# Performance work log

Hardware: AMD Instinct MI355X
Metric: run time of the kernel (lower is better)

Reference implementation:

```python
import jax, jax.numpy as jnp
import numpy as np
import math

BS, SEQ, HID = 1, 2048, 2048
NH, NKV, HD = 32, 8, 64
BASE = 10000.0


def rotate_half(x):
    x1, x2 = x[..., : x.shape[-1] // 2], x[..., x.shape[-1] // 2 :]
    return jnp.concatenate((-x2, x1), axis=-1)


def setup_inputs() -> dict:
    key = jax.random.key(0)
    ks = jax.random.split(key, 6)
    s = 0.02
    return {
        "x": jax.random.normal(ks[0], (BS, SEQ, HID), dtype=jnp.float32),
        "attention_mask": jnp.zeros((BS, SEQ), dtype=jnp.float32),
        "position_ids": jnp.broadcast_to(jnp.arange(SEQ, dtype=jnp.int64 if jax.config.jax_enable_x64 else jnp.int32), (BS, SEQ)),
        "wq": jax.random.normal(ks[1], (HID, NH * HD), dtype=jnp.float32) * s,
        "wk": jax.random.normal(ks[2], (HID, NKV * HD), dtype=jnp.float32) * s,
        "wv": jax.random.normal(ks[3], (HID, NKV * HD), dtype=jnp.float32) * s,
        "wo": jax.random.normal(ks[4], (NH * HD, HID), dtype=jnp.float32) * s,
    }


def reference(x, attention_mask, position_ids, wq, wk, wv, wo):
    bs, seq, _ = x.shape
    groups = NH // NKV

    q = (x @ wq).reshape(bs, seq, NH, HD).transpose(0, 2, 1, 3)   # [b,H,S,D]
    k = (x @ wk).reshape(bs, seq, NKV, HD).transpose(0, 2, 1, 3)  # [b,Hkv,S,D]
    v = (x @ wv).reshape(bs, seq, NKV, HD).transpose(0, 2, 1, 3)

    # rotary embedding
    inv_freq = 1.0 / (BASE ** (jnp.arange(0, HD, 2, dtype=jnp.float32) / HD))  # [D/2]
    freqs = position_ids.astype(jnp.float32)[:, :, None] * inv_freq[None, None, :]  # [b,S,D/2]
    emb = jnp.concatenate((freqs, freqs), axis=-1)               # [b,S,D]
    cos = jnp.cos(emb)[:, None, :, :].astype(x.dtype)            # [b,1,S,D]
    sin = jnp.sin(emb)[:, None, :, :].astype(x.dtype)
    q = q * cos + rotate_half(q) * sin
    k = k * cos + rotate_half(k) * sin

    # repeat_kv (GQA expand)
    k = jnp.repeat(k, groups, axis=1)  # [b,H,S,D]
    v = jnp.repeat(v, groups, axis=1)

    scores = jnp.einsum("bhqd,bhkd->bhqk", q, k) / math.sqrt(HD)
    scores = scores + attention_mask[:, None, None, :]
    attn = jax.nn.softmax(scores.astype(jnp.float32), axis=-1).astype(q.dtype)
    out = jnp.einsum("bhqk,bhkd->bhqd", attn, v)                 # [b,H,S,D]
    out = out.transpose(0, 2, 1, 3).reshape(bs, seq, NH * HD)
    return out @ wo
```

## Files before the change

### kernel.cpp

```cpp
#include <hip/hip_runtime.h>

#define SEQ 2048
#define HID 2048
#define NH  32
#define NKV 8
#define HD  64

typedef _Float16 f16;
typedef __attribute__((ext_vector_type(4))) _Float16 f16x4;
typedef __attribute__((ext_vector_type(8))) _Float16 f16x8;
typedef __attribute__((ext_vector_type(2))) __fp16   h16x2;
typedef __attribute__((ext_vector_type(4))) float    f32x4;

__device__ __forceinline__ f32x4 mfma_16x16x32(f16x8 a, f16x8 b, f32x4 c) {
    return __builtin_amdgcn_mfma_f32_16x16x32_f16(a, b, c, 0, 0, 0);
}

__device__ __forceinline__ void async16(const void* g, void* l) {
    __builtin_amdgcn_global_load_lds(
        (const __attribute__((address_space(1))) void*)g,
        (__attribute__((address_space(3))) void*)l,
        16, 0, 0);
}

__device__ __forceinline__ void xcd_colmap(int& bx, int& by) {
    int gx = gridDim.x, gy = gridDim.y;
    int nwg = gx * gy;
    int orig = by * gx + bx;
    int q = nwg >> 3, r = nwg & 7;
    int xcd = orig & 7, loc = orig >> 3;
    int wg = (xcd < r ? xcd * (q + 1) : r * (q + 1) + (xcd - r) * q) + loc;
    bx = wg / gy;
    by = wg - bx * gy;
}

__global__ void prep_all(const float* __restrict__ x,
                         const float* __restrict__ wq, const float* __restrict__ wk,
                         const float* __restrict__ wv, const float* __restrict__ wo,
                         f16* __restrict__ xb,
                         f16* __restrict__ Wcat, f16* __restrict__ woT) {
    __shared__ float ft[64 * 65];
    int z = blockIdx.z;
    int tid = threadIdx.x;
    if (z == 4) {
        int base = (blockIdx.y * 32 + blockIdx.x) * 4096 + tid * 8;
#pragma unroll
        for (int i = 0; i < 2; i++) {
            int off = base + i * 2048;
            float4 a = *(const float4*)(x + off);
            float4 b = *(const float4*)(x + off + 4);
            f16x8 o = { (f16)a.x, (f16)a.y, (f16)a.z, (f16)a.w,
                        (f16)b.x, (f16)b.y, (f16)b.z, (f16)b.w };
            *(f16x8*)(xb + off) = o;
        }
        return;
    }
    const float* src; f16* dst; int C;
    if      (z == 0) { src = wq; dst = Wcat;                         C = 2048; }
    else if (z == 1) { src = wk; dst = Wcat + (size_t)2048 * 2048;   C = 512;  }
    else if (z == 2) { src = wv; dst = Wcat + (size_t)2560 * 2048;   C = 512;  }
    else             { src = wo; dst = woT;                          C = 2048; }
    int c0 = blockIdx.x * 64, r0 = blockIdx.y * 64;
    if (c0 >= C) return;
    int c4 = tid & 15;
#pragma unroll
    for (int i = 0; i < 4; i++) {
        int r = (tid >> 4) * 4 + i;
        float4 v = *(const float4*)(src + (size_t)(r0 + r) * C + c0 + c4 * 4);
        *(float4*)(&ft[r * 65 + c4 * 4]) = v;
    }
    __syncthreads();
    int q = tid & 7;
#pragma unroll
    for (int it = 0; it < 2; it++) {
        int jj = (tid >> 3) + it * 32;
        f16x8 v;
#pragma unroll
        for (int e = 0; e < 8; e++)
            v[e] = (f16)ft[(q * 8 + e) * 65 + jj];
        *(f16x8*)(dst + (size_t)(c0 + jj) * 2048 + r0 + q * 8) = v;
    }
}

template <int MODE, int BM>
__global__ __launch_bounds__(256)
void gemm_bt(const f16* __restrict__ A, const f16* __restrict__ BT,
             float* __restrict__ Cf, f16* __restrict__ Q, f16* __restrict__ Kk,
             f16* __restrict__ VT, const int* __restrict__ pos,
             const float* __restrict__ mask, int N, int K) {
    constexpr int MI = BM / 32;
    constexpr int AR = BM / 4;
    __shared__ f16 As[2][BM * 64];
    __shared__ f16 Bs[2][128 * 64];
    int t = threadIdx.x;
    int w = t >> 6, lane = t & 63, quad = lane >> 4, l15 = lane & 15;
    int wm = w >> 1, wn = w & 1;
    int bx = blockIdx.x, by = blockIdx.y;
    xcd_colmap(bx, by);
    int m0 = by * BM, n0 = bx * 128;
    int sw = l15 & 7;

    int r8 = lane >> 3;
    int cc = (lane & 7) ^ r8;
    const f16* Ag = A  + (size_t)(m0 + w * AR + r8) * K + cc * 8;
    const f16* Bg = BT + (size_t)(n0 + w * 32 + r8) * K + cc * 8;

    f32x4 acc[MI][4] = {};

#pragma unroll
    for (int a = 0; a < AR / 8; a++)
        async16(Ag + (size_t)(8 * a) * K, &As[0][(w * AR + 8 * a) * 64]);
#pragma unroll
    for (int g = 0; g < 4; g++)
        async16(Bg + (size_t)(8 * g) * K, &Bs[0][(w * 32 + 8 * g) * 64]);
    __syncthreads();

    int b = 0;
    for (int kt = 64; kt <= K; kt += 64) {
        if (kt < K) {
#pragma unroll
            for (int a = 0; a < AR / 8; a++)
                async16(Ag + (size_t)(8 * a) * K + kt, &As[b ^ 1][(w * AR + 8 * a) * 64]);
#pragma unroll
            for (int g = 0; g < 4; g++)
                async16(Bg + (size_t)(8 * g) * K + kt, &Bs[b ^ 1][(w * 32 + 8 * g) * 64]);
        }
        f16x8 af[MI][2], bf[4][2];
#pragma unroll
        for (int mi = 0; mi < MI; mi++) {
            int row = wm * (BM / 2) + mi * 16 + l15;
#pragma unroll
            for (int kh = 0; kh < 2; kh++)
                af[mi][kh] = *(const f16x8*)(&As[b][row * 64 + ((kh * 4 + quad) ^ sw) * 8]);
        }
#pragma unroll
        for (int ni = 0; ni < 4; ni++) {
            int row = wn * 64 + ni * 16 + l15;
#pragma unroll
            for (int kh = 0; kh < 2; kh++)
                bf[ni][kh] = *(const f16x8*)(&Bs[b][row * 64 + ((kh * 4 + quad) ^ sw) * 8]);
        }
#pragma unroll
        for (int mi = 0; mi < MI; mi++)
#pragma unroll
            for (int ni = 0; ni < 4; ni++) {
                acc[mi][ni] = mfma_16x16x32(af[mi][0], bf[ni][0], acc[mi][ni]);
                acc[mi][ni] = mfma_16x16x32(af[mi][1], bf[ni][1], acc[mi][ni]);
            }
        __syncthreads();
        b ^= 1;
    }

    int rb  = m0 + wm * (BM / 2) + quad * 4;
    int cbh = n0 + wn * 64;
    if (MODE == 0) {
        if (cbh < (NH + NKV) * HD) {
            bool isQ = cbh < NH * HD;
            f16* dst = isQ ? (Q  + (size_t)(cbh >> 6) * SEQ * HD)
                           : (Kk + (size_t)((cbh - NH * HD) >> 6) * SEQ * HD);
            float scale = isQ ? 0.18033688011112042f : 1.0f;
            float fr[2];
#pragma unroll
            for (int ni = 0; ni < 2; ni++)
                fr[ni] = __builtin_amdgcn_exp2f(
                    (float)(ni * 16 + l15) * -0.41524101186092029f);
#pragma unroll
            for (int mi = 0; mi < MI; mi++)
#pragma unroll
                for (int r = 0; r < 4; r++) {
                    int row = rb + mi * 16 + r;
                    float pv = (float)pos[row];
#pragma unroll
                    for (int ni = 0; ni < 2; ni++) {
                        float sn, cs;
                        __sincosf(pv * fr[ni], &sn, &cs);
                        float x1 = acc[mi][ni][r], x2 = acc[mi][ni + 2][r];
                        int d = ni * 16 + l15;
                        dst[(size_t)row * HD + d]      = (f16)(scale * (x1 * cs - x2 * sn));
                        dst[(size_t)row * HD + d + 32] = (f16)(scale * (x2 * cs + x1 * sn));
                    }
                }
        } else {
            const float LOG2E = 1.4426950408889634f;
#pragma unroll
            for (int mi = 0; mi < MI; mi++) {
                float4 mv = *(const float4*)(mask + rb + mi * 16);
                float em[4];
#pragma unroll
                for (int r = 0; r < 4; r++)
                    em[r] = __builtin_amdgcn_exp2f((&mv.x)[r] * LOG2E);
#pragma unroll
                for (int ni = 0; ni < 4; ni++) {
                    int c2 = cbh - (NH + NKV) * HD + ni * 16 + l15;
                    f16x4 v4;
                    ((h16x2*)&v4)[0] = __builtin_amdgcn_cvt_pkrtz(
                        acc[mi][ni][0] * em[0], acc[mi][ni][1] * em[1]);
                    ((h16x2*)&v4)[1] = __builtin_amdgcn_cvt_pkrtz(
                        acc[mi][ni][2] * em[2], acc[mi][ni][3] * em[3]);
                    *(f16x4*)(VT + (size_t)c2 * SEQ + rb + mi * 16) = v4;
                }
            }
        }
    } else {
#pragma unroll
        for (int mi = 0; mi < MI; mi++)
#pragma unroll
            for (int ni = 0; ni < 4; ni++)
#pragma unroll
                for (int r = 0; r < 4; r++)
                    Cf[(size_t)(rb + mi * 16 + r) * N + cbh + ni * 16 + l15] =
                        acc[mi][ni][r];
    }
}

__global__ __launch_bounds__(512)
void attn_fused(const f16* __restrict__ Qb, const f16* __restrict__ Kb,
                const f16* __restrict__ VTb, const float* __restrict__ mask,
                f16* __restrict__ ctx) {
    __shared__ f16 Ks[3][64 * 64];
    __shared__ f16 Vs[3][64 * 64];
    __shared__ f16 Em[SEQ];

    int t = threadIdx.x, w = t >> 6, lane = t & 63, quad = lane >> 4, l15 = lane & 15;
    int h = blockIdx.y, kvh = h >> 2;
    int qbase = blockIdx.x * 256 + w * 32;
    const f16* Qh = Qb  + (size_t)h   * SEQ * HD;
    const f16* Kh = Kb  + (size_t)kvh * SEQ * HD;
    const f16* Vh = VTb + (size_t)kvh * HD * SEQ;
    int sw = l15 & 7;
    const float LOG2E = 1.4426950408889634f;

    int r8 = lane >> 3;
    int cc = (lane & 7) ^ r8;
    bool isK = w < 4;
    int ws = isK ? w : (w - 4);
    const f16* g0;
    long gstep;
    if (isK) {
        int gk = 32 * (ws >> 1) + 4 * (ws & 1) + 8 * (r8 >> 2) + (r8 & 3);
        g0 = Kh + (size_t)gk * HD + cc * 8;
        gstep = (long)16 * HD;
    } else {
        g0 = Vh + (size_t)(ws * 16 + r8) * SEQ + cc * 8;
        gstep = (long)8 * SEQ;
    }
    const f16* g1 = g0 + gstep;
    long adv = isK ? (long)64 * HD : 64;
    int lr0 = ws * 16 * 64, lr1 = lr0 + 8 * 64;

    f16 *kA = &Ks[0][0], *kB = &Ks[1][0], *kC3 = &Ks[2][0];
    f16 *vA = &Vs[0][0], *vB = &Vs[1][0], *vC3 = &Vs[2][0];

    {
        f16* dst = isK ? kA : vA;
        async16(g0, dst + lr0);
        async16(g1, dst + lr1);
    }

    {
        int idx = t * 4;
        float4 mv = *(const float4*)(mask + idx);
        f16x4 e;
        ((h16x2*)&e)[0] = __builtin_amdgcn_cvt_pkrtz(
            __builtin_amdgcn_exp2f(mv.x * LOG2E), __builtin_amdgcn_exp2f(mv.y * LOG2E));
        ((h16x2*)&e)[1] = __builtin_amdgcn_cvt_pkrtz(
            __builtin_amdgcn_exp2f(mv.z * LOG2E), __builtin_amdgcn_exp2f(mv.w * LOG2E));
        *(f16x4*)(&Em[idx]) = e;
    }

    f16x8 bq[2][2];
#pragma unroll
    for (int qg = 0; qg < 2; qg++)
#pragma unroll
        for (int ks = 0; ks < 2; ks++)
            bq[qg][ks] = *(const f16x8*)(Qh + (size_t)(qbase + qg * 16 + l15) * HD
                                            + ks * 32 + quad * 8);

    f32x4 o[4][2] = {};
    f32x4 ol[2]   = {};

    int c0 = (quad ^ sw) * 8, c1 = ((4 | quad) ^ sw) * 8;

    asm volatile("s_waitcnt lgkmcnt(0)" ::: "memory");

    const int NT = SEQ / 64;
    for (int ktl = 0; ktl < NT; ktl++) {
        if (ktl + 1 < NT) {
            g0 += adv; g1 += adv;
            f16* dst = (isK ? kB : vB);
            async16(g0, dst + lr0);
            async16(g1, dst + lr1);
            asm volatile("s_waitcnt vmcnt(4)" ::: "memory");
        } else {
            asm volatile("s_waitcnt vmcnt(0)" ::: "memory");
        }
        __builtin_amdgcn_sched_barrier(0);
        __builtin_amdgcn_s_barrier();
        __builtin_amdgcn_sched_barrier(0);

        const f16* Kb_ = kA;
        const f16* Vb_ = vA;

        f32x4 st[4][2] = {};
        __builtin_amdgcn_s_setprio(1);
#pragma unroll
        for (int ni = 0; ni < 4; ni++) {
            const f16* kr = Kb_ + (ni * 16 + l15) * 64;
            f16x8 ak0 = *(const f16x8*)(kr + c0);
            f16x8 ak1 = *(const f16x8*)(kr + c1);
#pragma unroll
            for (int qg = 0; qg < 2; qg++) {
                st[ni][qg] = mfma_16x16x32(ak0, bq[qg][0], st[ni][qg]);
                st[ni][qg] = mfma_16x16x32(ak1, bq[qg][1], st[ni][qg]);
            }
        }
        __builtin_amdgcn_s_setprio(0);
        f16x8 pb[2][2];
#pragma unroll
        for (int ni = 0; ni < 4; ni++)
#pragma unroll
            for (int qg = 0; qg < 2; qg++) {
                h16x2 lo = __builtin_amdgcn_cvt_pkrtz(
                    __builtin_amdgcn_exp2f(st[ni][qg][0]),
                    __builtin_amdgcn_exp2f(st[ni][qg][1]));
                h16x2 hi = __builtin_amdgcn_cvt_pkrtz(
                    __builtin_amdgcn_exp2f(st[ni][qg][2]),
                    __builtin_amdgcn_exp2f(st[ni][qg][3]));
                ((h16x2*)&pb[qg][ni >> 1])[(ni & 1) * 2]     = lo;
                ((h16x2*)&pb[qg][ni >> 1])[(ni & 1) * 2 + 1] = hi;
            }
        f16x8 em0 = *(const f16x8*)(&Em[ktl * 64 + quad * 8]);
        f16x8 em1 = *(const f16x8*)(&Em[ktl * 64 + 32 + quad * 8]);
        __builtin_amdgcn_s_setprio(1);
#pragma unroll
        for (int qg = 0; qg < 2; qg++) {
            ol[qg] = mfma_16x16x32(em0, pb[qg][0], ol[qg]);
            ol[qg] = mfma_16x16x32(em1, pb[qg][1], ol[qg]);
        }
#pragma unroll
        for (int dt = 0; dt < 4; dt++) {
            const f16* vr = Vb_ + (dt * 16 + l15) * 64;
            f16x8 av0 = *(const f16x8*)(vr + c0);
            f16x8 av1 = *(const f16x8*)(vr + c1);
#pragma unroll
            for (int qg = 0; qg < 2; qg++) {
                o[dt][qg] = mfma_16x16x32(av0, pb[qg][0], o[dt][qg]);
                o[dt][qg] = mfma_16x16x32(av1, pb[qg][1], o[dt][qg]);
            }
        }
        __builtin_amdgcn_s_setprio(0);
        f16* tk = kA; kA = kB; kB = kC3; kC3 = tk;
        f16* tv = vA; vA = vB; vB = vC3; vC3 = tv;
    }

    float inv[2] = { 1.0f / ol[0][0], 1.0f / ol[1][0] };
#pragma unroll
    for (int dt = 0; dt < 4; dt++)
#pragma unroll
        for (int qg = 0; qg < 2; qg++) {
            f16x4 v4;
            ((h16x2*)&v4)[0] = __builtin_amdgcn_cvt_pkrtz(
                o[dt][qg][0] * inv[qg], o[dt][qg][1] * inv[qg]);
            ((h16x2*)&v4)[1] = __builtin_amdgcn_cvt_pkrtz(
                o[dt][qg][2] * inv[qg], o[dt][qg][3] * inv[qg]);
            *(f16x4*)(ctx + (size_t)(qbase + qg * 16 + l15) * (NH * HD)
                          + h * HD + dt * 16 + quad * 4) = v4;
        }
}

extern "C" void kernel_launch(void* const* d_in, const int* in_sizes, int n_in,
                              void* d_out, int out_size, void* d_ws, size_t ws_size,
                              hipStream_t stream) {
    const float* x    = (const float*)d_in[0];
    const float* mask = (const float*)d_in[1];
    const int*   pos  = (const int*)  d_in[2];
    const float* wq   = (const float*)d_in[3];
    const float* wk   = (const float*)d_in[4];
    const float* wv   = (const float*)d_in[5];
    const float* wo   = (const float*)d_in[6];
    float* out = (float*)d_out;

    char* ws = (char*)d_ws;
    f16*   xb    = (f16*)(ws);
    f16*   Wcat  = (f16*)(ws + ((size_t)8  << 20));
    f16*   woT   = (f16*)(ws + ((size_t)20 << 20));
    f16*   Qb    = (f16*)(ws + ((size_t)28 << 20));
    f16*   Kb    = (f16*)(ws + ((size_t)36 << 20));
    f16*   VTb   = (f16*)(ws + ((size_t)38 << 20));
    f16*   ctx   = (f16*)(ws);

    prep_all<<<dim3(32, 32, 5), 256, 0, stream>>>(
        x, wq, wk, wv, wo, xb, Wcat, woT);

    gemm_bt<0, 64><<<dim3(3072 / 128, 2048 / 64), 256, 0, stream>>>(
        xb, Wcat, nullptr, Qb, Kb, VTb, pos, mask, 3072, 2048);

    attn_fused<<<dim3(SEQ / 256, NH), 512, 0, stream>>>(
        Qb, Kb, VTb, mask, ctx);

    gemm_bt<1, 64><<<dim3(2048 / 128, 2048 / 64), 256, 0, stream>>>(
        ctx, woT, out, nullptr, nullptr, nullptr, nullptr, nullptr, 2048, 2048);
}
```

Baseline: 206.1 us.

## Load K/V fragments directly from global memory, dropping LDS staging and barriers

The attention kernel no longer stages K and V tiles through a triple-buffered LDS ring with async global-to-LDS copies and per-tile block barriers. Each wave now loads its K and V MFMA fragments straight from global memory into registers every iteration, relying on L1/L2 to serve the data the eight waves share. Launch bounds now request two blocks per CU, which the smaller LDS footprint allows. The change removes the barrier synchronisation and LDS traffic, but it multiplies global/cache load traffic eightfold per block and exposes load latency that is no longer prefetched a tile ahead.

```diff
diff --git a/kernel.cpp b/kernel.cpp
--- a/kernel.cpp
+++ b/kernel.cpp
@@ -213,12 +213,10 @@
     }
 }
 
-__global__ __launch_bounds__(512)
+__global__ __launch_bounds__(512, 2)
 void attn_fused(const f16* __restrict__ Qb, const f16* __restrict__ Kb,
                 const f16* __restrict__ VTb, const float* __restrict__ mask,
                 f16* __restrict__ ctx) {
-    __shared__ f16 Ks[3][64 * 64];
-    __shared__ f16 Vs[3][64 * 64];
     __shared__ f16 Em[SEQ];
 
     int t = threadIdx.x, w = t >> 6, lane = t & 63, quad = lane >> 4, l15 = lane & 15;
@@ -227,35 +225,7 @@
     const f16* Qh = Qb  + (size_t)h   * SEQ * HD;
     const f16* Kh = Kb  + (size_t)kvh * SEQ * HD;
     const f16* Vh = VTb + (size_t)kvh * HD * SEQ;
-    int sw = l15 & 7;
     const float LOG2E = 1.4426950408889634f;
-
-    int r8 = lane >> 3;
-    int cc = (lane & 7) ^ r8;
-    bool isK = w < 4;
-    int ws = isK ? w : (w - 4);
-    const f16* g0;
-    long gstep;
-    if (isK) {
-        int gk = 32 * (ws >> 1) + 4 * (ws & 1) + 8 * (r8 >> 2) + (r8 & 3);
-        g0 = Kh + (size_t)gk * HD + cc * 8;
-        gstep = (long)16 * HD;
-    } else {
-        g0 = Vh + (size_t)(ws * 16 + r8) * SEQ + cc * 8;
-        gstep = (long)8 * SEQ;
-    }
-    const f16* g1 = g0 + gstep;
-    long adv = isK ? (long)64 * HD : 64;
-    int lr0 = ws * 16 * 64, lr1 = lr0 + 8 * 64;
-
-    f16 *kA = &Ks[0][0], *kB = &Ks[1][0], *kC3 = &Ks[2][0];
-    f16 *vA = &Vs[0][0], *vB = &Vs[1][0], *vC3 = &Vs[2][0];
-
-    {
-        f16* dst = isK ? kA : vA;
-        async16(g0, dst + lr0);
-        async16(g1, dst + lr1);
-    }
 
     {
         int idx = t * 4;
@@ -279,41 +249,40 @@
     f32x4 o[4][2] = {};
     f32x4 ol[2]   = {};
 
-    int c0 = (quad ^ sw) * 8, c1 = ((4 | quad) ^ sw) * 8;
-
-    asm volatile("s_waitcnt lgkmcnt(0)" ::: "memory");
-
-    const int NT = SEQ / 64;
-    for (int ktl = 0; ktl < NT; ktl++) {
-        if (ktl + 1 < NT) {
-            g0 += adv; g1 += adv;
-            f16* dst = (isK ? kB : vB);
-            async16(g0, dst + lr0);
-            async16(g1, dst + lr1);
-            asm volatile("s_waitcnt vmcnt(4)" ::: "memory");
-        } else {
-            asm volatile("s_waitcnt vmcnt(0)" ::: "memory");
-        }
-        __builtin_amdgcn_sched_barrier(0);
-        __builtin_amdgcn_s_barrier();
-        __builtin_amdgcn_sched_barrier(0);
-
-        const f16* Kb_ = kA;
-        const f16* Vb_ = vA;
-
+    int gkb = 8 * (l15 >> 2) + (l15 & 3);
+    const f16* Kl = Kh + (size_t)gkb * HD + quad * 8;
+    const f16* Vl = Vh + (size_t)l15 * SEQ + quad * 8;
+
+    __syncthreads();
+
+#pragma unroll 1
+    for (int ktl = 0; ktl < SEQ / 64; ktl++) {
+        int key0 = ktl * 64;
+        f16x8 vf[4][2];
+#pragma unroll
+        for (int dt = 0; dt < 4; dt++)
+#pragma unroll
+            for (int kh = 0; kh < 2; kh++)
+                vf[dt][kh] = *(const f16x8*)(Vl + (size_t)(dt * 16) * SEQ
+                                                + key0 + kh * 32);
+        f16x8 kf[4][2];
+#pragma unroll
+        for (int ni = 0; ni < 4; ni++) {
+            const int nio = (ni >> 1) * 32 + (ni & 1) * 4;
+#pragma unroll
+            for (int kh = 0; kh < 2; kh++)
+                kf[ni][kh] = *(const f16x8*)(Kl + (size_t)(key0 + nio) * HD
+                                                + kh * 32);
+        }
         f32x4 st[4][2] = {};
         __builtin_amdgcn_s_setprio(1);
 #pragma unroll
-        for (int ni = 0; ni < 4; ni++) {
-            const f16* kr = Kb_ + (ni * 16 + l15) * 64;
-            f16x8 ak0 = *(const f16x8*)(kr + c0);
-            f16x8 ak1 = *(const f16x8*)(kr + c1);
+        for (int ni = 0; ni < 4; ni++)
 #pragma unroll
             for (int qg = 0; qg < 2; qg++) {
-                st[ni][qg] = mfma_16x16x32(ak0, bq[qg][0], st[ni][qg]);
-                st[ni][qg] = mfma_16x16x32(ak1, bq[qg][1], st[ni][qg]);
-            }
-        }
+                st[ni][qg] = mfma_16x16x32(kf[ni][0], bq[qg][0], st[ni][qg]);
+                st[ni][qg] = mfma_16x16x32(kf[ni][1], bq[qg][1], st[ni][qg]);
+            }
         __builtin_amdgcn_s_setprio(0);
         f16x8 pb[2][2];
 #pragma unroll
@@ -329,8 +298,8 @@
                 ((h16x2*)&pb[qg][ni >> 1])[(ni & 1) * 2]     = lo;
                 ((h16x2*)&pb[qg][ni >> 1])[(ni & 1) * 2 + 1] = hi;
             }
-        f16x8 em0 = *(const f16x8*)(&Em[ktl * 64 + quad * 8]);
-        f16x8 em1 = *(const f16x8*)(&Em[ktl * 64 + 32 + quad * 8]);
+        f16x8 em0 = *(const f16x8*)(&Em[key0 + quad * 8]);
+        f16x8 em1 = *(const f16x8*)(&Em[key0 + 32 + quad * 8]);
         __builtin_amdgcn_s_setprio(1);
 #pragma unroll
         for (int qg = 0; qg < 2; qg++) {
@@ -338,19 +307,13 @@
             ol[qg] = mfma_16x16x32(em1, pb[qg][1], ol[qg]);
         }
 #pragma unroll
-        for (int dt = 0; dt < 4; dt++) {
-            const f16* vr = Vb_ + (dt * 16 + l15) * 64;
-            f16x8 av0 = *(const f16x8*)(vr + c0);
-            f16x8 av1 = *(const f16x8*)(vr + c1);
+        for (int dt = 0; dt < 4; dt++)
 #pragma unroll
             for (int qg = 0; qg < 2; qg++) {
-                o[dt][qg] = mfma_16x16x32(av0, pb[qg][0], o[dt][qg]);
-                o[dt][qg] = mfma_16x16x32(av1, pb[qg][1], o[dt][qg]);
-            }
-        }
+                o[dt][qg] = mfma_16x16x32(vf[dt][0], pb[qg][0], o[dt][qg]);
+                o[dt][qg] = mfma_16x16x32(vf[dt][1], pb[qg][1], o[dt][qg]);
+            }
         __builtin_amdgcn_s_setprio(0);
-        f16* tk = kA; kA = kB; kB = kC3; kC3 = tk;
-        f16* tv = vA; vA = vB; vB = vC3; vC3 = tv;
     }
 
     float inv[2] = { 1.0f / ol[0][0], 1.0f / ol[1][0] };
```

New measurement: 282.6 us. 1.37x slower.

## Specialize attention warps into producer loaders and 64-row consumer computers

Applied to the files above, without the earlier changes.

Warps in the fused attention kernel are split into roles: four producer warps issue all async K/V tile loads into LDS, and four consumer warps each compute 64 query rows instead of 32. Launch bounds now request two blocks per CU. The aim is to separate memory issue from MFMA work and give each computing warp more reuse of each K/V fragment it reads from LDS. The cost is that half the warps do no math, consumer register pressure roughly doubles, and the vmcnt(4) wait now covers four loads per producer, which may weaken prefetch depth.

```diff
diff --git a/kernel.cpp b/kernel.cpp
--- a/kernel.cpp
+++ b/kernel.cpp
@@ -213,7 +213,7 @@
     }
 }
 
-__global__ __launch_bounds__(512)
+__global__ __launch_bounds__(512, 2)
 void attn_fused(const f16* __restrict__ Qb, const f16* __restrict__ Kb,
                 const f16* __restrict__ VTb, const float* __restrict__ mask,
                 f16* __restrict__ ctx) {
@@ -223,38 +223,44 @@
 
     int t = threadIdx.x, w = t >> 6, lane = t & 63, quad = lane >> 4, l15 = lane & 15;
     int h = blockIdx.y, kvh = h >> 2;
-    int qbase = blockIdx.x * 256 + w * 32;
     const f16* Qh = Qb  + (size_t)h   * SEQ * HD;
     const f16* Kh = Kb  + (size_t)kvh * SEQ * HD;
     const f16* Vh = VTb + (size_t)kvh * HD * SEQ;
     int sw = l15 & 7;
     const float LOG2E = 1.4426950408889634f;
+    bool isProd = w < 4;
 
     int r8 = lane >> 3;
     int cc = (lane & 7) ^ r8;
-    bool isK = w < 4;
-    int ws = isK ? w : (w - 4);
-    const f16* g0;
-    long gstep;
-    if (isK) {
-        int gk = 32 * (ws >> 1) + 4 * (ws & 1) + 8 * (r8 >> 2) + (r8 & 3);
-        g0 = Kh + (size_t)gk * HD + cc * 8;
-        gstep = (long)16 * HD;
-    } else {
-        g0 = Vh + (size_t)(ws * 16 + r8) * SEQ + cc * 8;
-        gstep = (long)8 * SEQ;
-    }
-    const f16* g1 = g0 + gstep;
-    long adv = isK ? (long)64 * HD : 64;
-    int lr0 = ws * 16 * 64, lr1 = lr0 + 8 * 64;
+    const f16 *kv0 = nullptr, *kv1 = nullptr, *kv2 = nullptr, *kv3 = nullptr;
+    long adv = 0;
+    int lbase = 0;
+    bool isK = w < 2;
+    if (isProd) {
+        if (isK) {
+            const f16* bl = Kh + (size_t)(w * 32 + 8 * (r8 >> 2) + (r8 & 3)) * HD
+                               + cc * 8;
+            kv0 = bl;                   kv1 = bl + (size_t)16 * HD;
+            kv2 = bl + (size_t)4 * HD;  kv3 = bl + (size_t)20 * HD;
+            adv = (long)64 * HD;
+            lbase = w * 32 * 64;
+        } else {
+            int ws2 = w - 2;
+            const f16* bl = Vh + (size_t)(ws2 * 32 + r8) * SEQ + cc * 8;
+            kv0 = bl;                    kv1 = bl + (size_t)8 * SEQ;
+            kv2 = bl + (size_t)16 * SEQ; kv3 = bl + (size_t)24 * SEQ;
+            adv = 64;
+            lbase = ws2 * 32 * 64;
+        }
+    }
 
     f16 *kA = &Ks[0][0], *kB = &Ks[1][0], *kC3 = &Ks[2][0];
     f16 *vA = &Vs[0][0], *vB = &Vs[1][0], *vC3 = &Vs[2][0];
 
-    {
-        f16* dst = isK ? kA : vA;
-        async16(g0, dst + lr0);
-        async16(g1, dst + lr1);
+    if (isProd) {
+        f16* dst = (isK ? kA : vA) + lbase;
+        async16(kv0, dst);        async16(kv1, dst + 512);
+        async16(kv2, dst + 1024); async16(kv3, dst + 1536);
     }
 
     {
@@ -268,16 +274,20 @@
         *(f16x4*)(&Em[idx]) = e;
     }
 
-    f16x8 bq[2][2];
-#pragma unroll
-    for (int qg = 0; qg < 2; qg++)
-#pragma unroll
-        for (int ks = 0; ks < 2; ks++)
-            bq[qg][ks] = *(const f16x8*)(Qh + (size_t)(qbase + qg * 16 + l15) * HD
-                                            + ks * 32 + quad * 8);
-
-    f32x4 o[4][2] = {};
-    f32x4 ol[2]   = {};
+    int cw = w - 4;
+    int qbase = blockIdx.x * 256 + cw * 64;
+    f16x8 bq[4][2];
+    if (!isProd) {
+#pragma unroll
+        for (int qg = 0; qg < 4; qg++)
+#pragma unroll
+            for (int ks = 0; ks < 2; ks++)
+                bq[qg][ks] = *(const f16x8*)(Qh
+                    + (size_t)(qbase + qg * 16 + l15) * HD + ks * 32 + quad * 8);
+    }
+
+    f32x4 o[4][4] = {};
+    f32x4 ol[4]   = {};
 
     int c0 = (quad ^ sw) * 8, c1 = ((4 | quad) ^ sw) * 8;
 
@@ -285,87 +295,95 @@
 
     const int NT = SEQ / 64;
     for (int ktl = 0; ktl < NT; ktl++) {
-        if (ktl + 1 < NT) {
-            g0 += adv; g1 += adv;
-            f16* dst = (isK ? kB : vB);
-            async16(g0, dst + lr0);
-            async16(g1, dst + lr1);
-            asm volatile("s_waitcnt vmcnt(4)" ::: "memory");
-        } else {
-            asm volatile("s_waitcnt vmcnt(0)" ::: "memory");
+        if (isProd) {
+            if (ktl + 1 < NT) {
+                kv0 += adv; kv1 += adv; kv2 += adv; kv3 += adv;
+                f16* dst = (isK ? kB : vB) + lbase;
+                async16(kv0, dst);        async16(kv1, dst + 512);
+                async16(kv2, dst + 1024); async16(kv3, dst + 1536);
+                asm volatile("s_waitcnt vmcnt(4)" ::: "memory");
+            } else {
+                asm volatile("s_waitcnt vmcnt(0)" ::: "memory");
+            }
         }
         __builtin_amdgcn_sched_barrier(0);
         __builtin_amdgcn_s_barrier();
         __builtin_amdgcn_sched_barrier(0);
 
-        const f16* Kb_ = kA;
-        const f16* Vb_ = vA;
-
-        f32x4 st[4][2] = {};
-        __builtin_amdgcn_s_setprio(1);
-#pragma unroll
-        for (int ni = 0; ni < 4; ni++) {
-            const f16* kr = Kb_ + (ni * 16 + l15) * 64;
-            f16x8 ak0 = *(const f16x8*)(kr + c0);
-            f16x8 ak1 = *(const f16x8*)(kr + c1);
-#pragma unroll
-            for (int qg = 0; qg < 2; qg++) {
-                st[ni][qg] = mfma_16x16x32(ak0, bq[qg][0], st[ni][qg]);
-                st[ni][qg] = mfma_16x16x32(ak1, bq[qg][1], st[ni][qg]);
-            }
-        }
-        __builtin_amdgcn_s_setprio(0);
-        f16x8 pb[2][2];
-#pragma unroll
-        for (int ni = 0; ni < 4; ni++)
-#pragma unroll
-            for (int qg = 0; qg < 2; qg++) {
-                h16x2 lo = __builtin_amdgcn_cvt_pkrtz(
-                    __builtin_amdgcn_exp2f(st[ni][qg][0]),
-                    __builtin_amdgcn_exp2f(st[ni][qg][1]));
-                h16x2 hi = __builtin_amdgcn_cvt_pkrtz(
-                    __builtin_amdgcn_exp2f(st[ni][qg][2]),
-                    __builtin_amdgcn_exp2f(st[ni][qg][3]));
-                ((h16x2*)&pb[qg][ni >> 1])[(ni & 1) * 2]     = lo;
-                ((h16x2*)&pb[qg][ni >> 1])[(ni & 1) * 2 + 1] = hi;
-            }
-        f16x8 em0 = *(const f16x8*)(&Em[ktl * 64 + quad * 8]);
-        f16x8 em1 = *(const f16x8*)(&Em[ktl * 64 + 32 + quad * 8]);
-        __builtin_amdgcn_s_setprio(1);
-#pragma unroll
-        for (int qg = 0; qg < 2; qg++) {
-            ol[qg] = mfma_16x16x32(em0, pb[qg][0], ol[qg]);
-            ol[qg] = mfma_16x16x32(em1, pb[qg][1], ol[qg]);
-        }
-#pragma unroll
-        for (int dt = 0; dt < 4; dt++) {
-            const f16* vr = Vb_ + (dt * 16 + l15) * 64;
-            f16x8 av0 = *(const f16x8*)(vr + c0);
-            f16x8 av1 = *(const f16x8*)(vr + c1);
-#pragma unroll
-            for (int qg = 0; qg < 2; qg++) {
-                o[dt][qg] = mfma_16x16x32(av0, pb[qg][0], o[dt][qg]);
-                o[dt][qg] = mfma_16x16x32(av1, pb[qg][1], o[dt][qg]);
-            }
-        }
-        __builtin_amdgcn_s_setprio(0);
+        if (!isProd) {
+            const f16* Kb_ = kA;
+            const f16* Vb_ = vA;
+
+            f32x4 st[4][4] = {};
+            __builtin_amdgcn_s_setprio(1);
+#pragma unroll
+            for (int ni = 0; ni < 4; ni++) {
+                const f16* kr = Kb_ + (ni * 16 + l15) * 64;
+                f16x8 ak0 = *(const f16x8*)(kr + c0);
+                f16x8 ak1 = *(const f16x8*)(kr + c1);
+#pragma unroll
+                for (int qg = 0; qg < 4; qg++) {
+                    st[ni][qg] = mfma_16x16x32(ak0, bq[qg][0], st[ni][qg]);
+                    st[ni][qg] = mfma_16x16x32(ak1, bq[qg][1], st[ni][qg]);
+                }
+            }
+            __builtin_amdgcn_s_setprio(0);
+            f16x8 pb[4][2];
+#pragma unroll
+            for (int ni = 0; ni < 4; ni++)
+#pragma unroll
+                for (int qg = 0; qg < 4; qg++) {
+                    h16x2 lo = __builtin_amdgcn_cvt_pkrtz(
+                        __builtin_amdgcn_exp2f(st[ni][qg][0]),
+                        __builtin_amdgcn_exp2f(st[ni][qg][1]));
+                    h16x2 hi = __builtin_amdgcn_cvt_pkrtz(
+                        __builtin_amdgcn_exp2f(st[ni][qg][2]),
+                        __builtin_amdgcn_exp2f(st[ni][qg][3]));
+                    ((h16x2*)&pb[qg][ni >> 1])[(ni & 1) * 2]     = lo;
+                    ((h16x2*)&pb[qg][ni >> 1])[(ni & 1) * 2 + 1] = hi;
+                }
+            f16x8 em0 = *(const f16x8*)(&Em[ktl * 64 + quad * 8]);
+            f16x8 em1 = *(const f16x8*)(&Em[ktl * 64 + 32 + quad * 8]);
+            __builtin_amdgcn_s_setprio(1);
+#pragma unroll
+            for (int qg = 0; qg < 4; qg++) {
+                ol[qg] = mfma_16x16x32(em0, pb[qg][0], ol[qg]);
+                ol[qg] = mfma_16x16x32(em1, pb[qg][1], ol[qg]);
+            }
+#pragma unroll
+            for (int dt = 0; dt < 4; dt++) {
+                const f16* vr = Vb_ + (dt * 16 + l15) * 64;
+                f16x8 av0 = *(const f16x8*)(vr + c0);
+                f16x8 av1 = *(const f16x8*)(vr + c1);
+#pragma unroll
+                for (int qg = 0; qg < 4; qg++) {
+                    o[dt][qg] = mfma_16x16x32(av0, pb[qg][0], o[dt][qg]);
+                    o[dt][qg] = mfma_16x16x32(av1, pb[qg][1], o[dt][qg]);
+                }
+            }
+            __builtin_amdgcn_s_setprio(0);
+        }
         f16* tk = kA; kA = kB; kB = kC3; kC3 = tk;
         f16* tv = vA; vA = vB; vB = vC3; vC3 = tv;
     }
 
-    float inv[2] = { 1.0f / ol[0][0], 1.0f / ol[1][0] };
-#pragma unroll
-    for (int dt = 0; dt < 4; dt++)
-#pragma unroll
-        for (int qg = 0; qg < 2; qg++) {
-            f16x4 v4;
-            ((h16x2*)&v4)[0] = __builtin_amdgcn_cvt_pkrtz(
-                o[dt][qg][0] * inv[qg], o[dt][qg][1] * inv[qg]);
-            ((h16x2*)&v4)[1] = __builtin_amdgcn_cvt_pkrtz(
-                o[dt][qg][2] * inv[qg], o[dt][qg][3] * inv[qg]);
-            *(f16x4*)(ctx + (size_t)(qbase + qg * 16 + l15) * (NH * HD)
-                          + h * HD + dt * 16 + quad * 4) = v4;
-        }
+    if (!isProd) {
+        float inv[4];
+#pragma unroll
+        for (int qg = 0; qg < 4; qg++) inv[qg] = 1.0f / ol[qg][0];
+#pragma unroll
+        for (int dt = 0; dt < 4; dt++)
+#pragma unroll
+            for (int qg = 0; qg < 4; qg++) {
+                f16x4 v4;
+                ((h16x2*)&v4)[0] = __builtin_amdgcn_cvt_pkrtz(
+                    o[dt][qg][0] * inv[qg], o[dt][qg][1] * inv[qg]);
+                ((h16x2*)&v4)[1] = __builtin_amdgcn_cvt_pkrtz(
+                    o[dt][qg][2] * inv[qg], o[dt][qg][3] * inv[qg]);
+                *(f16x4*)(ctx + (size_t)(qbase + qg * 16 + l15) * (NH * HD)
+                              + h * HD + dt * 16 + quad * 4) = v4;
+            }
+    }
 }
 
 extern "C" void kernel_launch(void* const* d_in, const int* in_sizes, int n_in,
```

After: 206.4 us. No clear change (+0.1%).

## Software-pipeline attention: overlap QK^T of current tile with PV of previous tile

Applied to the files above, without the earlier changes.

Restructures the attention main loop so each iteration computes QK^T and the softmax exponentials for tile k, while the P·V and row-sum MFMAs run on the probabilities from tile k-1. A final epilogue handles the last tile. K/V shared-memory buffers grow from three to four, indexed by iteration modulo 4, so the previous tile's V stays resident while the next tile loads; the load wait is tightened to vmcnt(2). The aim is to hide the exponential/convert latency behind MFMA work. The cost is more LDS per block, which may reduce how many blocks fit on a CU, plus extra registers for the carried probabilities.

```diff
diff --git a/kernel.cpp b/kernel.cpp
--- a/kernel.cpp
+++ b/kernel.cpp
@@ -217,8 +217,8 @@
 void attn_fused(const f16* __restrict__ Qb, const f16* __restrict__ Kb,
                 const f16* __restrict__ VTb, const float* __restrict__ mask,
                 f16* __restrict__ ctx) {
-    __shared__ f16 Ks[3][64 * 64];
-    __shared__ f16 Vs[3][64 * 64];
+    __shared__ f16 Ks[4][64 * 64];
+    __shared__ f16 Vs[4][64 * 64];
     __shared__ f16 Em[SEQ];
 
     int t = threadIdx.x, w = t >> 6, lane = t & 63, quad = lane >> 4, l15 = lane & 15;
@@ -248,11 +248,8 @@
     long adv = isK ? (long)64 * HD : 64;
     int lr0 = ws * 16 * 64, lr1 = lr0 + 8 * 64;
 
-    f16 *kA = &Ks[0][0], *kB = &Ks[1][0], *kC3 = &Ks[2][0];
-    f16 *vA = &Vs[0][0], *vB = &Vs[1][0], *vC3 = &Vs[2][0];
-
     {
-        f16* dst = isK ? kA : vA;
+        f16* dst = (isK ? &Ks[0][0] : &Vs[0][0]);
         async16(g0, dst + lr0);
         async16(g1, dst + lr1);
     }
@@ -278,6 +275,7 @@
 
     f32x4 o[4][2] = {};
     f32x4 ol[2]   = {};
+    f16x8 pbP[2][2];
 
     int c0 = (quad ^ sw) * 8, c1 = ((4 | quad) ^ sw) * 8;
 
@@ -287,10 +285,10 @@
     for (int ktl = 0; ktl < NT; ktl++) {
         if (ktl + 1 < NT) {
             g0 += adv; g1 += adv;
-            f16* dst = (isK ? kB : vB);
+            f16* dst = (isK ? &Ks[(ktl + 1) & 3][0] : &Vs[(ktl + 1) & 3][0]);
             async16(g0, dst + lr0);
             async16(g1, dst + lr1);
-            asm volatile("s_waitcnt vmcnt(4)" ::: "memory");
+            asm volatile("s_waitcnt vmcnt(2)" ::: "memory");
         } else {
             asm volatile("s_waitcnt vmcnt(0)" ::: "memory");
         }
@@ -298,8 +296,7 @@
         __builtin_amdgcn_s_barrier();
         __builtin_amdgcn_sched_barrier(0);
 
-        const f16* Kb_ = kA;
-        const f16* Vb_ = vA;
+        const f16* Kb_ = &Ks[ktl & 3][0];
 
         f32x4 st[4][2] = {};
         __builtin_amdgcn_s_setprio(1);
@@ -315,7 +312,31 @@
             }
         }
         __builtin_amdgcn_s_setprio(0);
-        f16x8 pb[2][2];
+
+        if (ktl > 0) {
+            const f16* Vb_ = &Vs[(ktl - 1) & 3][0];
+            f16x8 em0 = *(const f16x8*)(&Em[(ktl - 1) * 64 + quad * 8]);
+            f16x8 em1 = *(const f16x8*)(&Em[(ktl - 1) * 64 + 32 + quad * 8]);
+            __builtin_amdgcn_s_setprio(1);
+#pragma unroll
+            for (int qg = 0; qg < 2; qg++) {
+                ol[qg] = mfma_16x16x32(em0, pbP[qg][0], ol[qg]);
+                ol[qg] = mfma_16x16x32(em1, pbP[qg][1], ol[qg]);
+            }
+#pragma unroll
+            for (int dt = 0; dt < 4; dt++) {
+                const f16* vr = Vb_ + (dt * 16 + l15) * 64;
+                f16x8 av0 = *(const f16x8*)(vr + c0);
+                f16x8 av1 = *(const f16x8*)(vr + c1);
+#pragma unroll
+                for (int qg = 0; qg < 2; qg++) {
+                    o[dt][qg] = mfma_16x16x32(av0, pbP[qg][0], o[dt][qg]);
+                    o[dt][qg] = mfma_16x16x32(av1, pbP[qg][1], o[dt][qg]);
+                }
+            }
+            __builtin_amdgcn_s_setprio(0);
+        }
+
 #pragma unroll
         for (int ni = 0; ni < 4; ni++)
 #pragma unroll
@@ -326,16 +347,19 @@
                 h16x2 hi = __builtin_amdgcn_cvt_pkrtz(
                     __builtin_amdgcn_exp2f(st[ni][qg][2]),
                     __builtin_amdgcn_exp2f(st[ni][qg][3]));
-                ((h16x2*)&pb[qg][ni >> 1])[(ni & 1) * 2]     = lo;
-                ((h16x2*)&pb[qg][ni >> 1])[(ni & 1) * 2 + 1] = hi;
-            }
-        f16x8 em0 = *(const f16x8*)(&Em[ktl * 64 + quad * 8]);
-        f16x8 em1 = *(const f16x8*)(&Em[ktl * 64 + 32 + quad * 8]);
-        __builtin_amdgcn_s_setprio(1);
+                ((h16x2*)&pbP[qg][ni >> 1])[(ni & 1) * 2]     = lo;
+                ((h16x2*)&pbP[qg][ni >> 1])[(ni & 1) * 2 + 1] = hi;
+            }
+    }
+
+    {
+        const f16* Vb_ = &Vs[(NT - 1) & 3][0];
+        f16x8 em0 = *(const f16x8*)(&Em[(NT - 1) * 64 + quad * 8]);
+        f16x8 em1 = *(const f16x8*)(&Em[(NT - 1) * 64 + 32 + quad * 8]);
 #pragma unroll
         for (int qg = 0; qg < 2; qg++) {
-            ol[qg] = mfma_16x16x32(em0, pb[qg][0], ol[qg]);
-            ol[qg] = mfma_16x16x32(em1, pb[qg][1], ol[qg]);
+            ol[qg] = mfma_16x16x32(em0, pbP[qg][0], ol[qg]);
+            ol[qg] = mfma_16x16x32(em1, pbP[qg][1], ol[qg]);
         }
 #pragma unroll
         for (int dt = 0; dt < 4; dt++) {
@@ -344,13 +368,10 @@
             f16x8 av1 = *(const f16x8*)(vr + c1);
 #pragma unroll
             for (int qg = 0; qg < 2; qg++) {
-                o[dt][qg] = mfma_16x16x32(av0, pb[qg][0], o[dt][qg]);
-                o[dt][qg] = mfma_16x16x32(av1, pb[qg][1], o[dt][qg]);
-            }
-        }
-        __builtin_amdgcn_s_setprio(0);
-        f16* tk = kA; kA = kB; kB = kC3; kC3 = tk;
-        f16* tv = vA; vA = vB; vB = vC3; vC3 = tv;
+                o[dt][qg] = mfma_16x16x32(av0, pbP[qg][0], o[dt][qg]);
+                o[dt][qg] = mfma_16x16x32(av1, pbP[qg][1], o[dt][qg]);
+            }
+        }
     }
 
     float inv[2] = { 1.0f / ol[0][0], 1.0f / ol[1][0] };
```

Measured after the change: 204.6 us. About the same (-0.7%).
